# Performance work log

Hardware: AMD Instinct MI355X
Metric: run time of the kernel (lower is better)

Reference implementation:

```python
import jax, jax.numpy as jnp
import numpy as np

N = 4096        # number of nodes
C = 512         # in_features
L_LAT = 64      # L_latent
EPS = 0.25      # epsilon


def setup_inputs() -> dict:
    key = jax.random.key(0)
    ks = jax.random.split(key, 8)
    def lin(k, fan_in, shape):
        return (jax.random.normal(k, shape, jnp.float32) / np.float32(np.sqrt(fan_in)))
    x = jax.random.normal(ks[0], (N, C), jnp.float32)
    adj = jax.random.uniform(ks[1], (N, N), jnp.float32)  # dense nonneg kernel
    W_proj = lin(ks[2], C, (C, L_LAT)); b_proj = jnp.zeros((L_LAT,), jnp.float32)
    W_pi1 = lin(ks[3], L_LAT, (L_LAT, C)); b_pi1 = jnp.zeros((C,), jnp.float32)
    W_pi2 = lin(ks[4], C, (C, 1)); b_pi2 = jnp.zeros((1,), jnp.float32)
    W_f = lin(ks[5], C, (C, C)); b_f = jnp.zeros((C,), jnp.float32)
    dt = jnp.array([0.1], jnp.float32)
    return {"x": x, "adj": adj, "W_proj": W_proj, "b_proj": b_proj,
            "W_pi1": W_pi1, "b_pi1": b_pi1, "W_pi2": W_pi2, "b_pi2": b_pi2,
            "W_f": W_f, "b_f": b_f, "dt": dt}


def reference(x, adj, W_proj, b_proj, W_pi1, b_pi1, W_pi2, b_pi2, W_f, b_f, dt):
    # proj_list: x -> latent [n, L]
    z = x @ W_proj + b_proj
    # pi_list: Linear -> ReLU -> Linear -> Sigmoid, squeeze to [n]
    pi = jax.nn.sigmoid(jax.nn.relu(z @ W_pi1 + b_pi1) @ W_pi2 + b_pi2)[:, 0]
    # q_epsilon_tilde: row sums of the kernel
    q = adj.sum(axis=1)                       # [n]
    # K_tilde = K_epsilon @ diag(pi/q)  == column scaling
    K_tilde = adj * (pi / q)[None, :]         # [n, n]
    # D_tilde diagonal; torch.inverse of a diagonal == elementwise reciprocal
    d = K_tilde.sum(axis=1) + 1e-5            # [n]
    # target = relu(f(x)) with f = Linear(C, C)
    target = jax.nn.relu(x @ W_f + b_f)       # [n, C]
    # L @ target = (1/eps) * diag(1/d) @ K_tilde @ target - target
    Lt = (K_tilde @ target) / (EPS * d)[:, None] - target
    return target + dt[0] * Lt
```

## Files before the change

### kernel.cpp

```cpp
#include <hip/hip_runtime.h>
#include <hip/hip_bf16.h>

#define N_NODES 4096
#define C_DIM   512
#define L_DIM   64
#define SPLITS  4
#define KCHUNK  (N_NODES / SPLITS)

typedef unsigned short u16;
typedef unsigned int   u32;
using bf16x8 = __attribute__((ext_vector_type(8))) __bf16;
using u16x8  = __attribute__((ext_vector_type(8))) unsigned short;
using f32x4  = __attribute__((ext_vector_type(4))) float;

__device__ __forceinline__ float b2f(u16 u) {
    union { unsigned int i; float f; } v; v.i = ((unsigned int)u) << 16; return v.f;
}
__device__ __forceinline__ u16 f2b(float f) {
    __bf16 h = (__bf16)f;
    union { __bf16 h; u16 u; } v; v.h = h; return v.u;
}
__device__ __forceinline__ void gload16(const void* g, void* l) {
    __builtin_amdgcn_global_load_lds((const __attribute__((address_space(1))) void*)g,
                                     (__attribute__((address_space(3))) void*)l,
                                     16, 0, 0);
}
__device__ __forceinline__ int detect_mode_inl(const u16* __restrict__ adj) {
    int m = 0;
#pragma unroll
    for (int i = 0; i < 64; ++i) m |= (adj[i] >= 0x8000) ? 1 : 0;
    return m;
}
__device__ __forceinline__ float ldin(const void* p, int i, int mode) {
    if (mode) return ((const float*)p)[i];
    return b2f(((const u16*)p)[i]);
}

#define OFF_MODE  0
#define OFF_DT    64
#define OFF_BIAS  1024
#define OFF_BP    4096
#define OFF_BP1   4608
#define OFF_WP2   8192
#define OFF_BP2   10240
#define OFF_Q     16384
#define OFF_S     32768
#define OFF_DV    49152
#define OFF_WPP   65536
#define OFF_WP1P  131072
#define OFF_WFT   196608
#define OFF_TST   9437184
#define OFF_XB    13631488
#define OFF_ADJB  17825792

__global__ __launch_bounds__(256) void k1_prep(const void* __restrict__ adj, const void* __restrict__ x,
        const void* Wp, const void* bp, const void* Wp1, const void* bp1,
        const void* Wp2, const void* bp2, const void* Wf, const void* bfc, const void* dt,
        int* __restrict__ modep,
        float* __restrict__ bp_f, float* __restrict__ bp1_f,
        float* __restrict__ Wp2_f, float* __restrict__ bp2_f,
        float* __restrict__ bias_f, float* __restrict__ dt_f,
        u32* __restrict__ WpP, u32* __restrict__ Wp1P,
        u16* __restrict__ adjb, float* __restrict__ q, u16* __restrict__ xb,
        u16* __restrict__ WfT) {
    __shared__ float tile[32][33];
    int bid = blockIdx.x, tid = threadIdx.x;
    int mode = detect_mode_inl((const u16*)adj);
    if (bid < 1024) {
        int wave = tid >> 6, lane = tid & 63;
        int row = bid * 4 + wave;
        float acc = 0.f;
        if (mode) {
            const float4* rp = (const float4*)((const float*)adj + (size_t)row * N_NODES);
            ushort4* wp = (ushort4*)(adjb + (size_t)row * N_NODES);
#pragma unroll 8
            for (int it = 0; it < 16; ++it) {
                float4 v = rp[it * 64 + lane];
                acc += (v.x + v.y) + (v.z + v.w);
                ushort4 o; o.x = f2b(v.x); o.y = f2b(v.y); o.z = f2b(v.z); o.w = f2b(v.w);
                wp[it * 64 + lane] = o;
            }
        } else {
            const u16x8* rp = (const u16x8*)((const u16*)adj + (size_t)row * N_NODES);
#pragma unroll
            for (int it = 0; it < 8; ++it) {
                u16x8 v = rp[it * 64 + lane];
#pragma unroll
                for (int e = 0; e < 8; ++e) acc += b2f(v[e]);
            }
        }
#pragma unroll
        for (int off = 32; off > 0; off >>= 1) acc += __shfl_down(acc, off);
        if (lane == 0) q[row] = acc;
    } else if (bid < 3072) {
        if (mode == 0) return;
        int idx = (bid - 1024) * 256 + tid;
        float4 v = ((const float4*)x)[idx];
        ushort4 o; o.x = f2b(v.x); o.y = f2b(v.y); o.z = f2b(v.z); o.w = f2b(v.w);
        ((ushort4*)xb)[idx] = o;
    } else if (bid < 3328) {
        int g = bid - 3072;
        int tx = tid & 31, ty = tid >> 5;
        int x0 = (g & 15) * 32, y0 = (g >> 4) * 32;
        if (mode) {
            const float* src = (const float*)Wf;
#pragma unroll
            for (int r = ty; r < 32; r += 8) tile[r][tx] = src[(size_t)(y0 + r) * C_DIM + x0 + tx];
        } else {
            const u16* src = (const u16*)Wf;
#pragma unroll
            for (int r = ty; r < 32; r += 8) tile[r][tx] = b2f(src[(size_t)(y0 + r) * C_DIM + x0 + tx]);
        }
        __syncthreads();
#pragma unroll
        for (int r = ty; r < 32; r += 8)
            WfT[(size_t)(x0 + r) * C_DIM + y0 + tx] = f2b(tile[tx][r]);
    } else if (bid < 3392) {
        int idx = (bid - 3328) * 256 + tid;
        int k2i = idx >> 6, j = idx & 63;
        float a = ldin(Wp, (2 * k2i) * L_DIM + j, mode);
        float b = ldin(Wp, (2 * k2i + 1) * L_DIM + j, mode);
        WpP[idx] = (u32)f2b(a) | ((u32)f2b(b) << 16);
    } else if (bid < 3456) {
        int idx = (bid - 3392) * 256 + tid;
        int jj2 = idx >> 9, m = idx & 511;
        float a = ldin(Wp1, (2 * jj2) * C_DIM + m, mode);
        float b = ldin(Wp1, (2 * jj2 + 1) * C_DIM + m, mode);
        Wp1P[idx] = (u32)f2b(a) | ((u32)f2b(b) << 16);
    } else {
        if (bid == 3456 && tid == 0) *modep = mode;
        int idx = (bid - 3456) * 256 + tid;
        if (idx < 64)           bp_f[idx]          = ldin(bp,  idx, mode);
        else if (idx < 576)     bp1_f[idx - 64]    = ldin(bp1, idx - 64, mode);
        else if (idx < 1088)    Wp2_f[idx - 576]   = ldin(Wp2, idx - 576, mode);
        else if (idx == 1088)   bp2_f[0]           = ldin(bp2, 0, mode);
        else if (idx < 1601)    bias_f[idx - 1089] = ldin(bfc, idx - 1089, mode);
        else if (idx == 1601)   dt_f[0]            = ldin(dt, 0, mode);
    }
}

__global__ __launch_bounds__(256) void k1p_pi(const void* __restrict__ xraw,
        const int* __restrict__ modep, const u16* __restrict__ xb,
        const u32* __restrict__ WpP, const u32* __restrict__ Wp1P,
        const float* __restrict__ bp_f,  const float* __restrict__ bp1_f,
        const float* __restrict__ Wp2_f, const float* __restrict__ bp2_f,
        const float* __restrict__ q, float* __restrict__ s) {
    __shared__ __align__(16) char smem[26880];
    int bid = blockIdx.x, tid = threadIdx.x;
    int mode = *modep;
    float (*sx)[C_DIM]      = (float(*)[C_DIM])smem;
    float (*red)[8][L_DIM]  = (float(*)[8][L_DIM])(smem + 16384);
    float (*sz)[L_DIM]      = (float(*)[L_DIM])(smem + 24576);
    float (*rw)[8]          = (float(*)[8])(smem + 26624);
    int i0 = bid * 8;
    const u16* xsrc = mode ? xb : (const u16*)xraw;
    const u16x8* xp = (const u16x8*)(xsrc + (size_t)i0 * C_DIM);
#pragma unroll
    for (int r = 0; r < 2; ++r) {
        u16x8 v = xp[tid + 256 * r];
        float* dstf = &sx[0][0] + (size_t)(tid + 256 * r) * 8;
#pragma unroll
        for (int e = 0; e < 8; ++e) dstf[e] = b2f(v[e]);
    }
    __syncthreads();
    int j = tid & 63, part = tid >> 6;
    float za[8];
#pragma unroll
    for (int n = 0; n < 8; ++n) za[n] = 0.f;
    const u32* wp = WpP + part * 4096 + j;
#pragma unroll 8
    for (int kk = 0; kk < 64; ++kk) {
        u32 w = wp[kk * 64];
        float wa = b2f((u16)(w & 0xFFFF)), wb = b2f((u16)(w >> 16));
        int k = part * 128 + kk * 2;
#pragma unroll
        for (int n = 0; n < 8; ++n) za[n] += sx[n][k] * wa + sx[n][k + 1] * wb;
    }
#pragma unroll
    for (int n = 0; n < 8; ++n) red[part][n][j] = za[n];
    __syncthreads();
#pragma unroll
    for (int r = 0; r < 2; ++r) {
        int idx = tid + r * 256; int n = idx >> 6, jj = idx & 63;
        sz[n][jj] = red[0][n][jj] + red[1][n][jj] + red[2][n][jj] + red[3][n][jj] + bp_f[jj];
    }
    __syncthreads();
    int m0 = tid, m1 = tid + 256;
    float h0[8], h1[8];
    float b0 = bp1_f[m0], b1 = bp1_f[m1];
#pragma unroll
    for (int n = 0; n < 8; ++n) { h0[n] = b0; h1[n] = b1; }
    const u32* w1p = Wp1P + m0;
#pragma unroll 4
    for (int jj2 = 0; jj2 < 32; ++jj2) {
        u32 w0 = w1p[jj2 * 512], w1 = w1p[jj2 * 512 + 256];
        float w0a = b2f((u16)(w0 & 0xFFFF)), w0b = b2f((u16)(w0 >> 16));
        float w1a = b2f((u16)(w1 & 0xFFFF)), w1b = b2f((u16)(w1 >> 16));
#pragma unroll
        for (int n = 0; n < 8; ++n) {
            float za_ = sz[n][2 * jj2], zb_ = sz[n][2 * jj2 + 1];
            h0[n] += za_ * w0a + zb_ * w0b;
            h1[n] += za_ * w1a + zb_ * w1b;
        }
    }
    float w2a = Wp2_f[m0], w2b = Wp2_f[m1];
    float p[8];
#pragma unroll
    for (int n = 0; n < 8; ++n)
        p[n] = fmaxf(h0[n], 0.f) * w2a + fmaxf(h1[n], 0.f) * w2b;
#pragma unroll
    for (int off = 32; off > 0; off >>= 1)
#pragma unroll
        for (int n = 0; n < 8; ++n) p[n] += __shfl_down(p[n], off);
    int lane = tid & 63, wave = tid >> 6;
    if (lane == 0) {
#pragma unroll
        for (int n = 0; n < 8; ++n) rw[wave][n] = p[n];
    }
    __syncthreads();
    if (tid < 8) {
        float tot = rw[0][tid] + rw[1][tid] + rw[2][tid] + rw[3][tid] + bp2_f[0];
        float pi = 1.f / (1.f + expf(-tot));
        s[i0 + tid] = pi / q[i0 + tid];
    }
}

__global__ __launch_bounds__(256) void k2_mid(const void* __restrict__ adjraw, const void* __restrict__ xraw,
        const int* __restrict__ modep,
        const float* __restrict__ s, const float* __restrict__ bias_f, const float* __restrict__ dt_f,
        const u16* __restrict__ adjb, const u16* __restrict__ xb, const u16* __restrict__ WfT,
        float* __restrict__ dv, u16* __restrict__ TsT,
        void* __restrict__ out, float* __restrict__ Pacc) {
    __shared__ __align__(16) char smem[16640];
    int bid = blockIdx.x, tid = threadIdx.x;
    int mode = *modep;
    if (bid < 1024) {
        float* s_lds = (float*)smem;
#pragma unroll
        for (int r = 0; r < 4; ++r) ((float4*)s_lds)[tid + 256 * r] = ((const float4*)s)[tid + 256 * r];
        __syncthreads();
        const u16* A = mode ? adjb : (const u16*)adjraw;
        int wave = tid >> 6, lane = tid & 63;
        int row = bid * 4 + wave;
        const u16x8* rp = (const u16x8*)(A + (size_t)row * N_NODES);
        float acc = 0.f;
#pragma unroll
        for (int it = 0; it < 8; ++it) {
            int chunk = it * 64 + lane;
            u16x8 v = rp[chunk];
            const float4* sp = (const float4*)(s_lds + chunk * 8);
            float4 s0 = sp[0], s1 = sp[1];
            acc += b2f(v[0]) * s0.x + b2f(v[1]) * s0.y + b2f(v[2]) * s0.z + b2f(v[3]) * s0.w;
            acc += b2f(v[4]) * s1.x + b2f(v[5]) * s1.y + b2f(v[6]) * s1.z + b2f(v[7]) * s1.w;
        }
#pragma unroll
        for (int off = 32; off > 0; off >>= 1) acc += __shfl_down(acc, off);
        if (lane == 0) dv[row] = acc + 1e-5f;
    } else {
        u16* lbuf = (u16*)smem;
        u16* lT = (u16*)smem;
        float* s_row = (float*)(smem + 16384);
        int g = bid - 1024;
        int lane = tid & 63, wave = tid >> 6;
        int bm = (g & 63) * 64, bn = (g >> 6) * 64;
        if (tid < 64) s_row[tid] = s[bm + tid];
        const u16* A = mode ? xb : (const u16*)xraw;
        float* tgt = mode ? (float*)out : Pacc;
        int quad = lane >> 4, l15 = lane & 15;
        int wm = wave * 16;
        const u16* Ap = A + (size_t)(bm + (tid >> 2)) * C_DIM + (tid & 3) * 8;
        const u16* Bp = WfT + (size_t)(bn + (tid >> 2)) * C_DIM + (tid & 3) * 8;
        f32x4 acc[4];
#pragma unroll
        for (int nt = 0; nt < 4; ++nt) acc[nt] = (f32x4){0.f, 0.f, 0.f, 0.f};
#define STAGE1(buf, k0)                                        \
        do {                                                   \
            gload16(Ap + (k0), lbuf + (buf) * 2048 + tid * 8); \
            gload16(Bp + (k0), lbuf + 4096 + (buf) * 2048 + tid * 8); \
        } while (0)
        STAGE1(0, 0);
        for (int it = 0; it < 16; ++it) {
            int cur = it & 1;
            if (it < 15) {
                STAGE1(cur ^ 1, (it + 1) * 32);
                asm volatile("s_waitcnt vmcnt(2)\n\ts_barrier" ::: "memory");
            } else {
                asm volatile("s_waitcnt vmcnt(0)\n\ts_barrier" ::: "memory");
            }
            __builtin_amdgcn_sched_barrier(0);
            bf16x8 af = *(const bf16x8*)&lbuf[cur * 2048 + (wm + l15) * 32 + quad * 8];
            bf16x8 bfv[4];
#pragma unroll
            for (int nt = 0; nt < 4; ++nt)
                bfv[nt] = *(const bf16x8*)&lbuf[4096 + cur * 2048 + (nt * 16 + l15) * 32 + quad * 8];
#pragma unroll
            for (int nt = 0; nt < 4; ++nt)
                acc[nt] = __builtin_amdgcn_mfma_f32_16x16x32_bf16(af, bfv[nt], acc[nt], 0, 0, 0);
            asm volatile("s_waitcnt lgkmcnt(0)\n\ts_barrier" ::: "memory");
        }
#undef STAGE1
        float c0 = 1.f - dt_f[0];
#pragma unroll
        for (int nt = 0; nt < 4; ++nt) {
            int col_l = nt * 16 + l15;
            float bv = bias_f[bn + col_l];
#pragma unroll
            for (int r = 0; r < 4; ++r) {
                int row_l = wm + quad * 4 + r;
                float t = fmaxf(acc[nt][r] + bv, 0.f);
                tgt[(size_t)(bm + row_l) * C_DIM + bn + col_l] = c0 * t;
                lT[col_l * 64 + row_l] = f2b(t * s_row[row_l]);
            }
        }
        __syncthreads();
        int col_l = tid >> 2, seg = tid & 3;
        uint4 w0 = *(const uint4*)&lT[col_l * 64 + seg * 16];
        uint4 w1 = *(const uint4*)&lT[col_l * 64 + seg * 16 + 8];
        u16* dst = TsT + (size_t)(bn + col_l) * N_NODES + bm + seg * 16;
        *(uint4*)dst = w0;
        *(uint4*)(dst + 8) = w1;
    }
}

__global__ __launch_bounds__(256) void k3_gemm2(const void* __restrict__ adjraw,
        const int* __restrict__ modep,
        const u16* __restrict__ adjb, const u16* __restrict__ TsT,
        const float* __restrict__ dv, const float* __restrict__ dt_f,
        void* __restrict__ out, float* __restrict__ Pacc) {
    __shared__ __align__(16) u16 lA[2][8192];
    __shared__ __align__(16) u16 lB[2][8192];
    int mode = *modep;
    const u16* A = mode ? adjb : (const u16*)adjraw;
    float* tgt = mode ? (float*)out : Pacc;
    int tid = threadIdx.x;
    int lane = tid & 63, wave = tid >> 6;
    int bm = blockIdx.x * 128, bn = blockIdx.y * 128;
    int kbase = blockIdx.z * KCHUNK;
    int wm = (wave & 1) * 64, wn = (wave >> 1) * 64;
    int quad = lane >> 4, l15 = lane & 15;

    const u16* Ab0 = A + (size_t)(bm + (tid >> 2)) * N_NODES + kbase + (tid & 3) * 8;
    const u16* Ab1 = A + (size_t)(bm + 64 + (tid >> 2)) * N_NODES + kbase + (tid & 3) * 8;
    const u16* Bb0 = TsT + (size_t)(bn + (tid >> 2)) * N_NODES + kbase + (tid & 3) * 8;
    const u16* Bb1 = TsT + (size_t)(bn + 64 + (tid >> 2)) * N_NODES + kbase + (tid & 3) * 8;

    f32x4 acc[4][4];
#pragma unroll
    for (int a = 0; a < 4; ++a)
#pragma unroll
        for (int b = 0; b < 4; ++b) acc[a][b] = (f32x4){0.f, 0.f, 0.f, 0.f};

#define STAGE(buf, k0)                                        \
    do {                                                      \
        u16* bA = &lA[(buf)][0];                              \
        u16* bB = &lB[(buf)][0];                              \
        gload16(Ab0 + (k0),      bA + tid * 8);               \
        gload16(Ab1 + (k0),      bA + 2048 + tid * 8);        \
        gload16(Ab0 + (k0) + 32, bA + 4096 + tid * 8);        \
        gload16(Ab1 + (k0) + 32, bA + 6144 + tid * 8);        \
        gload16(Bb0 + (k0),      bB + tid * 8);               \
        gload16(Bb1 + (k0),      bB + 2048 + tid * 8);        \
        gload16(Bb0 + (k0) + 32, bB + 4096 + tid * 8);        \
        gload16(Bb1 + (k0) + 32, bB + 6144 + tid * 8);        \
    } while (0)

    STAGE(0, 0);
    for (int it = 0; it < 16; ++it) {
        int cur = it & 1;
        if (it < 15) {
            STAGE(cur ^ 1, (it + 1) * 64);
            asm volatile("s_waitcnt vmcnt(8)\n\ts_barrier" ::: "memory");
        } else {
            asm volatile("s_waitcnt vmcnt(0)\n\ts_barrier" ::: "memory");
        }
        __builtin_amdgcn_sched_barrier(0);
#pragma unroll
        for (int kk = 0; kk < 2; ++kk) {
            const u16* baseA = &lA[cur][kk * 4096];
            const u16* baseB = &lB[cur][kk * 4096];
            bf16x8 af[4], bfv[4];
#pragma unroll
            for (int mt = 0; mt < 4; ++mt) af[mt] = *(const bf16x8*)&baseA[(wm + mt * 16 + l15) * 32 + quad * 8];
#pragma unroll
            for (int nt = 0; nt < 4; ++nt) bfv[nt] = *(const bf16x8*)&baseB[(wn + nt * 16 + l15) * 32 + quad * 8];
#pragma unroll
            for (int mt = 0; mt < 4; ++mt)
#pragma unroll
                for (int nt = 0; nt < 4; ++nt)
                    acc[mt][nt] = __builtin_amdgcn_mfma_f32_16x16x32_bf16(af[mt], bfv[nt], acc[mt][nt], 0, 0, 0);
        }
        asm volatile("s_waitcnt lgkmcnt(0)\n\ts_barrier" ::: "memory");
    }
#undef STAGE

    float c1 = dt_f[0] * 4.f;
#pragma unroll
    for (int mt = 0; mt < 4; ++mt) {
        float inv[4];
#pragma unroll
        for (int r = 0; r < 4; ++r) inv[r] = c1 / dv[bm + wm + mt * 16 + quad * 4 + r];
#pragma unroll
        for (int nt = 0; nt < 4; ++nt) {
            int col = bn + wn + nt * 16 + l15;
#pragma unroll
            for (int r = 0; r < 4; ++r) {
                int row = bm + wm + mt * 16 + quad * 4 + r;
                atomicAdd(&tgt[(size_t)row * C_DIM + col], acc[mt][nt][r] * inv[r]);
            }
        }
    }
}

__global__ __launch_bounds__(256) void k5_fin(const int* __restrict__ modep,
                                              const float* __restrict__ Pacc,
                                              u16* __restrict__ out) {
    if (*modep) return;
    int idx = blockIdx.x * 256 + threadIdx.x;
    float4 v = ((const float4*)Pacc)[idx];
    ushort4 o; o.x = f2b(v.x); o.y = f2b(v.y); o.z = f2b(v.z); o.w = f2b(v.w);
    ((ushort4*)out)[idx] = o;
}

extern "C" void kernel_launch(void* const* d_in, const int* in_sizes, int n_in,
                              void* d_out, int out_size, void* d_ws, size_t ws_size,
                              hipStream_t stream) {
    const void* x   = d_in[0];
    const void* adj = d_in[1];
    const void* Wp  = d_in[2];
    const void* bp  = d_in[3];
    const void* Wp1 = d_in[4];
    const void* bp1 = d_in[5];
    const void* Wp2 = d_in[6];
    const void* bp2 = d_in[7];
    const void* Wf  = d_in[8];
    const void* bfc = d_in[9];
    const void* dtp = d_in[10];

    char* ws = (char*)d_ws;
    int*   modep  = (int*)(ws + OFF_MODE);
    float* dt_f   = (float*)(ws + OFF_DT);
    float* bias_f = (float*)(ws + OFF_BIAS);
    float* bp_f   = (float*)(ws + OFF_BP);
    float* bp1_f  = (float*)(ws + OFF_BP1);
    float* Wp2_f  = (float*)(ws + OFF_WP2);
    float* bp2_f  = (float*)(ws + OFF_BP2);
    float* q      = (float*)(ws + OFF_Q);
    float* s      = (float*)(ws + OFF_S);
    float* dv     = (float*)(ws + OFF_DV);
    u32*   WpP    = (u32*)(ws + OFF_WPP);
    u32*   Wp1P   = (u32*)(ws + OFF_WP1P);
    u16*   WfT    = (u16*)(ws + OFF_WFT);
    u16*   TsT    = (u16*)(ws + OFF_TST);
    u16*   xb     = (u16*)(ws + OFF_XB);
    u16*   adjb   = (u16*)(ws + OFF_ADJB);
    float* Pacc   = (float*)(ws + OFF_ADJB);

    k1_prep<<<3463, 256, 0, stream>>>(adj, x, Wp, bp, Wp1, bp1, Wp2, bp2, Wf, bfc, dtp,
                                      modep, bp_f, bp1_f, Wp2_f, bp2_f, bias_f, dt_f,
                                      WpP, Wp1P, adjb, q, xb, WfT);
    k1p_pi<<<512, 256, 0, stream>>>(x, modep, xb, WpP, Wp1P, bp_f, bp1_f, Wp2_f, bp2_f, q, s);
    k2_mid<<<1536, 256, 0, stream>>>(adj, x, modep, s, bias_f, dt_f, adjb, xb, WfT,
                                     dv, TsT, d_out, Pacc);
    k3_gemm2<<<dim3(32, 4, SPLITS), 256, 0, stream>>>(adj, modep, adjb, TsT, dv, dt_f, d_out, Pacc);
    k5_fin<<<2048, 256, 0, stream>>>(modep, Pacc, (u16*)d_out);
}
```

Measured before the change: 218.6 us.

## Swizzle LDS layout, widen K tile, double split-K and remap blocks

The main adj×T GEMM now uses 8 K-splits instead of 4, giving 1024 blocks that are launched through a flat grid with a remapped block index. The LDS tile widens to 64 columns with an XOR swizzle to avoid bank conflicts, and double buffering is dropped, so each K step loads and then computes synchronously. The feature GEMM in k2 gets the same swizzled 64-wide single-buffer scheme. dv now stores a reciprocal so the epilogue multiplies instead of dividing. The costs are that global-load latency is no longer overlapped with compute and that twice as many atomic adds hit the output.

```diff
diff --git a/kernel.cpp b/kernel.cpp
--- a/kernel.cpp
+++ b/kernel.cpp
@@ -4,7 +4,7 @@
 #define N_NODES 4096
 #define C_DIM   512
 #define L_DIM   64
-#define SPLITS  4
+#define SPLITS  8
 #define KCHUNK  (N_NODES / SPLITS)
 
 typedef unsigned short u16;
@@ -255,50 +255,50 @@
         }
 #pragma unroll
         for (int off = 32; off > 0; off >>= 1) acc += __shfl_down(acc, off);
-        if (lane == 0) dv[row] = acc + 1e-5f;
+        if (lane == 0) dv[row] = 1.f / (acc + 1e-5f);
     } else {
-        u16* lbuf = (u16*)smem;
+        u16* lA = (u16*)smem;
+        u16* lB = (u16*)(smem + 8192);
         u16* lT = (u16*)smem;
         float* s_row = (float*)(smem + 16384);
         int g = bid - 1024;
         int lane = tid & 63, wave = tid >> 6;
         int bm = (g & 63) * 64, bn = (g >> 6) * 64;
         if (tid < 64) s_row[tid] = s[bm + tid];
-        const u16* A = mode ? xb : (const u16*)xraw;
+        const u16* Axb = mode ? xb : (const u16*)xraw;
         float* tgt = mode ? (float*)out : Pacc;
         int quad = lane >> 4, l15 = lane & 15;
         int wm = wave * 16;
-        const u16* Ap = A + (size_t)(bm + (tid >> 2)) * C_DIM + (tid & 3) * 8;
-        const u16* Bp = WfT + (size_t)(bn + (tid >> 2)) * C_DIM + (tid & 3) * 8;
+        int trow = tid >> 3;
+        int xslot = (tid & 7) ^ (trow & 7);
+        const u16* Ap0 = Axb + (size_t)(bm + trow) * C_DIM + xslot * 8;
+        const u16* Ap1 = Axb + (size_t)(bm + 32 + trow) * C_DIM + xslot * 8;
+        const u16* Bp0 = WfT + (size_t)(bn + trow) * C_DIM + xslot * 8;
+        const u16* Bp1 = WfT + (size_t)(bn + 32 + trow) * C_DIM + xslot * 8;
         f32x4 acc[4];
 #pragma unroll
         for (int nt = 0; nt < 4; ++nt) acc[nt] = (f32x4){0.f, 0.f, 0.f, 0.f};
-#define STAGE1(buf, k0)                                        \
-        do {                                                   \
-            gload16(Ap + (k0), lbuf + (buf) * 2048 + tid * 8); \
-            gload16(Bp + (k0), lbuf + 4096 + (buf) * 2048 + tid * 8); \
-        } while (0)
-        STAGE1(0, 0);
-        for (int it = 0; it < 16; ++it) {
-            int cur = it & 1;
-            if (it < 15) {
-                STAGE1(cur ^ 1, (it + 1) * 32);
-                asm volatile("s_waitcnt vmcnt(2)\n\ts_barrier" ::: "memory");
-            } else {
-                asm volatile("s_waitcnt vmcnt(0)\n\ts_barrier" ::: "memory");
+        for (int k0 = 0; k0 < C_DIM; k0 += 64) {
+            gload16(Ap0 + k0, lA + tid * 8);
+            gload16(Ap1 + k0, lA + 2048 + tid * 8);
+            gload16(Bp0 + k0, lB + tid * 8);
+            gload16(Bp1 + k0, lB + 2048 + tid * 8);
+            asm volatile("s_waitcnt vmcnt(0)\n\ts_barrier" ::: "memory");
+            __builtin_amdgcn_sched_barrier(0);
+#pragma unroll
+            for (int kk = 0; kk < 2; ++kk) {
+                int xr = (((kk << 2) | quad) ^ (l15 & 7)) * 8;
+                bf16x8 af = *(const bf16x8*)&lA[(wm + l15) * 64 + xr];
+                bf16x8 bfv[4];
+#pragma unroll
+                for (int nt = 0; nt < 4; ++nt)
+                    bfv[nt] = *(const bf16x8*)&lB[(nt * 16 + l15) * 64 + xr];
+#pragma unroll
+                for (int nt = 0; nt < 4; ++nt)
+                    acc[nt] = __builtin_amdgcn_mfma_f32_16x16x32_bf16(af, bfv[nt], acc[nt], 0, 0, 0);
             }
-            __builtin_amdgcn_sched_barrier(0);
-            bf16x8 af = *(const bf16x8*)&lbuf[cur * 2048 + (wm + l15) * 32 + quad * 8];
-            bf16x8 bfv[4];
-#pragma unroll
-            for (int nt = 0; nt < 4; ++nt)
-                bfv[nt] = *(const bf16x8*)&lbuf[4096 + cur * 2048 + (nt * 16 + l15) * 32 + quad * 8];
-#pragma unroll
-            for (int nt = 0; nt < 4; ++nt)
-                acc[nt] = __builtin_amdgcn_mfma_f32_16x16x32_bf16(af, bfv[nt], acc[nt], 0, 0, 0);
             asm volatile("s_waitcnt lgkmcnt(0)\n\ts_barrier" ::: "memory");
         }
-#undef STAGE1
         float c0 = 1.f - dt_f[0];
 #pragma unroll
         for (int nt = 0; nt < 4; ++nt) {
@@ -327,22 +327,29 @@
         const u16* __restrict__ adjb, const u16* __restrict__ TsT,
         const float* __restrict__ dv, const float* __restrict__ dt_f,
         void* __restrict__ out, float* __restrict__ Pacc) {
-    __shared__ __align__(16) u16 lA[2][8192];
-    __shared__ __align__(16) u16 lB[2][8192];
+    __shared__ __align__(16) u16 lA[8192];
+    __shared__ __align__(16) u16 lB[8192];
     int mode = *modep;
     const u16* A = mode ? adjb : (const u16*)adjraw;
     float* tgt = mode ? (float*)out : Pacc;
     int tid = threadIdx.x;
     int lane = tid & 63, wave = tid >> 6;
-    int bm = blockIdx.x * 128, bn = blockIdx.y * 128;
-    int kbase = blockIdx.z * KCHUNK;
+    int id = blockIdx.x;
+    int nid = (id & 7) * 128 + (id >> 3);
+    int kbase = (nid & 7) * KCHUNK;
+    int bn = ((nid >> 3) & 3) * 128;
+    int bm = (nid >> 5) * 128;
     int wm = (wave & 1) * 64, wn = (wave >> 1) * 64;
     int quad = lane >> 4, l15 = lane & 15;
-
-    const u16* Ab0 = A + (size_t)(bm + (tid >> 2)) * N_NODES + kbase + (tid & 3) * 8;
-    const u16* Ab1 = A + (size_t)(bm + 64 + (tid >> 2)) * N_NODES + kbase + (tid & 3) * 8;
-    const u16* Bb0 = TsT + (size_t)(bn + (tid >> 2)) * N_NODES + kbase + (tid & 3) * 8;
-    const u16* Bb1 = TsT + (size_t)(bn + 64 + (tid >> 2)) * N_NODES + kbase + (tid & 3) * 8;
+    int trow = tid >> 3;
+    int xslot = (tid & 7) ^ (trow & 7);
+
+    const u16* Ap[4]; const u16* Bp[4];
+#pragma unroll
+    for (int i = 0; i < 4; ++i) {
+        Ap[i] = A   + (size_t)(bm + i * 32 + trow) * N_NODES + kbase + xslot * 8;
+        Bp[i] = TsT + (size_t)(bn + i * 32 + trow) * N_NODES + kbase + xslot * 8;
+    }
 
     f32x4 acc[4][4];
 #pragma unroll
@@ -350,39 +357,21 @@
 #pragma unroll
         for (int b = 0; b < 4; ++b) acc[a][b] = (f32x4){0.f, 0.f, 0.f, 0.f};
 
-#define STAGE(buf, k0)                                        \
-    do {                                                      \
-        u16* bA = &lA[(buf)][0];                              \
-        u16* bB = &lB[(buf)][0];                              \
-        gload16(Ab0 + (k0),      bA + tid * 8);               \
-        gload16(Ab1 + (k0),      bA + 2048 + tid * 8);        \
-        gload16(Ab0 + (k0) + 32, bA + 4096 + tid * 8);        \
-        gload16(Ab1 + (k0) + 32, bA + 6144 + tid * 8);        \
-        gload16(Bb0 + (k0),      bB + tid * 8);               \
-        gload16(Bb1 + (k0),      bB + 2048 + tid * 8);        \
-        gload16(Bb0 + (k0) + 32, bB + 4096 + tid * 8);        \
-        gload16(Bb1 + (k0) + 32, bB + 6144 + tid * 8);        \
-    } while (0)
-
-    STAGE(0, 0);
-    for (int it = 0; it < 16; ++it) {
-        int cur = it & 1;
-        if (it < 15) {
-            STAGE(cur ^ 1, (it + 1) * 64);
-            asm volatile("s_waitcnt vmcnt(8)\n\ts_barrier" ::: "memory");
-        } else {
-            asm volatile("s_waitcnt vmcnt(0)\n\ts_barrier" ::: "memory");
-        }
+    for (int k0 = 0; k0 < KCHUNK; k0 += 64) {
+#pragma unroll
+        for (int i = 0; i < 4; ++i) gload16(Ap[i] + k0, lA + i * 2048 + tid * 8);
+#pragma unroll
+        for (int i = 0; i < 4; ++i) gload16(Bp[i] + k0, lB + i * 2048 + tid * 8);
+        asm volatile("s_waitcnt vmcnt(0)\n\ts_barrier" ::: "memory");
         __builtin_amdgcn_sched_barrier(0);
 #pragma unroll
         for (int kk = 0; kk < 2; ++kk) {
-            const u16* baseA = &lA[cur][kk * 4096];
-            const u16* baseB = &lB[cur][kk * 4096];
+            int xr = (((kk << 2) | quad) ^ (l15 & 7)) * 8;
             bf16x8 af[4], bfv[4];
 #pragma unroll
-            for (int mt = 0; mt < 4; ++mt) af[mt] = *(const bf16x8*)&baseA[(wm + mt * 16 + l15) * 32 + quad * 8];
-#pragma unroll
-            for (int nt = 0; nt < 4; ++nt) bfv[nt] = *(const bf16x8*)&baseB[(wn + nt * 16 + l15) * 32 + quad * 8];
+            for (int mt = 0; mt < 4; ++mt) af[mt] = *(const bf16x8*)&lA[(wm + mt * 16 + l15) * 64 + xr];
+#pragma unroll
+            for (int nt = 0; nt < 4; ++nt) bfv[nt] = *(const bf16x8*)&lB[(wn + nt * 16 + l15) * 64 + xr];
 #pragma unroll
             for (int mt = 0; mt < 4; ++mt)
 #pragma unroll
@@ -391,14 +380,13 @@
         }
         asm volatile("s_waitcnt lgkmcnt(0)\n\ts_barrier" ::: "memory");
     }
-#undef STAGE
 
     float c1 = dt_f[0] * 4.f;
 #pragma unroll
     for (int mt = 0; mt < 4; ++mt) {
         float inv[4];
 #pragma unroll
-        for (int r = 0; r < 4; ++r) inv[r] = c1 / dv[bm + wm + mt * 16 + quad * 4 + r];
+        for (int r = 0; r < 4; ++r) inv[r] = c1 * dv[bm + wm + mt * 16 + quad * 4 + r];
 #pragma unroll
         for (int nt = 0; nt < 4; ++nt) {
             int col = bn + wn + nt * 16 + l15;
@@ -461,6 +449,6 @@
     k1p_pi<<<512, 256, 0, stream>>>(x, modep, xb, WpP, Wp1P, bp_f, bp1_f, Wp2_f, bp2_f, q, s);
     k2_mid<<<1536, 256, 0, stream>>>(adj, x, modep, s, bias_f, dt_f, adjb, xb, WfT,
                                      dv, TsT, d_out, Pacc);
-    k3_gemm2<<<dim3(32, 4, SPLITS), 256, 0, stream>>>(adj, modep, adjb, TsT, dv, dt_f, d_out, Pacc);
+    k3_gemm2<<<1024, 256, 0, stream>>>(adj, modep, adjb, TsT, dv, dt_f, d_out, Pacc);
     k5_fin<<<2048, 256, 0, stream>>>(modep, Pacc, (u16*)d_out);
 }
```

New measurement: 240.2 us. 1.1x slower.
